# Performance work log

Hardware: AMD Instinct MI355X
Metric: run time of the kernel (lower is better)

Reference implementation:

```python
import jax, jax.numpy as jnp
import numpy as np

D_MODEL = 1024
NHEAD = 16
HEAD_DIM = D_MODEL // NHEAD
LN_EPS = 1e-5
ROPE_BASE = 10000.0


def _rope_cos_sin(n, head_dim):
    inv_freq = 1.0 / (ROPE_BASE ** (jnp.arange(0, head_dim, 2, dtype=jnp.float32) / head_dim))
    t = jnp.arange(n, dtype=jnp.float32)
    freqs = jnp.outer(t, inv_freq)  # (N, head_dim//2)
    return jnp.cos(freqs), jnp.sin(freqs)


def _apply_rope(x, cos, sin):
    # x: (B, H, N, hd); cos/sin: (N, hd//2)
    B, H, N, hd = x.shape
    xr = x.reshape(B, H, N, hd // 2, 2)
    x0, x1 = xr[..., 0], xr[..., 1]
    c = cos[None, None]
    s = sin[None, None]
    rot = jnp.stack([x0 * c - x1 * s, x0 * s + x1 * c], axis=-1)
    return rot.reshape(B, H, N, hd)


def setup_inputs() -> dict:
    key = jax.random.key(0)
    ks = jax.random.split(key, 6)
    D = D_MODEL
    scale = 1.0 / np.sqrt(D)
    x = jax.random.normal(ks[0], (2, 2048, D), dtype=jnp.float32)
    Wq = jax.random.normal(ks[1], (D, D), dtype=jnp.float32) * scale
    Wk = jax.random.normal(ks[2], (D, D), dtype=jnp.float32) * scale
    Wv = jax.random.normal(ks[3], (D, D), dtype=jnp.float32) * scale
    Wo = jax.random.normal(ks[4], (D, D), dtype=jnp.float32) * scale
    bq = jnp.zeros((D,), jnp.float32)
    bk = jnp.zeros((D,), jnp.float32)
    bv = jnp.zeros((D,), jnp.float32)
    bo = jnp.zeros((D,), jnp.float32)
    ln_w = jnp.ones((D,), jnp.float32)
    ln_b = jnp.zeros((D,), jnp.float32)
    return {"x": x, "ln_w": ln_w, "ln_b": ln_b, "Wq": Wq, "bq": bq,
            "Wk": Wk, "bk": bk, "Wv": Wv, "bv": bv, "Wo": Wo, "bo": bo}


def reference(x, ln_w, ln_b, Wq, bq, Wk, bk, Wv, bv, Wo, bo):
    B, N, D = x.shape
    H, hd = NHEAD, HEAD_DIM
    # LayerNorm
    mu = jnp.mean(x, axis=-1, keepdims=True)
    var = jnp.mean(jnp.square(x - mu), axis=-1, keepdims=True)
    xn = (x - mu) * jax.lax.rsqrt(var + LN_EPS) * ln_w + ln_b
    # QKV projections -> (B, H, N, hd)
    def proj(W, b):
        return (xn @ W.T + b).reshape(B, N, H, hd).transpose(0, 2, 1, 3)
    q = proj(Wq, bq)
    k = proj(Wk, bk)
    v = proj(Wv, bv)
    cos, sin = _rope_cos_sin(N, hd)
    q = _apply_rope(q, cos, sin)
    k = _apply_rope(k, cos, sin)
    scores = jnp.einsum('bhqd,bhkd->bhqk', q, k) / jnp.sqrt(jnp.float32(hd))
    attn = jax.nn.softmax(scores, axis=-1)
    out = jnp.einsum('bhqk,bhkd->bhqd', attn, v)
    out = out.transpose(0, 2, 1, 3).reshape(B, N, D)
    return x + out @ Wo.T + bo
```

## Files before the change

### kernel.cpp

```cpp
#include <hip/hip_runtime.h>


#define SEQ 2048
#define LN_EPS 1e-5f

using short8 = __attribute__((ext_vector_type(8))) short;
using f32x4  = __attribute__((ext_vector_type(4))) float;

__device__ __forceinline__ unsigned short f2bf(float f) {
  union { float f; unsigned u; } v; v.f = f;
  unsigned r = v.u + 0x7FFFu + ((v.u >> 16) & 1u);
  return (unsigned short)(r >> 16);
}

__device__ __forceinline__ void async16(const void* g, void* l) {
  __builtin_amdgcn_global_load_lds(
      (const __attribute__((address_space(1))) void*)g,
      (__attribute__((address_space(3))) void*)l, 16, 0, 0);
}

__global__ __launch_bounds__(256) void prep_kernel(
    const float* __restrict__ x, const float* __restrict__ lnw, const float* __restrict__ lnb,
    const float* __restrict__ wq, const float* __restrict__ wk,
    const float* __restrict__ wv, const float* __restrict__ wo,
    unsigned short* __restrict__ wqkv, unsigned short* __restrict__ wob,
    unsigned short* __restrict__ xn, float2* __restrict__ tab) {
  const int b = blockIdx.x, t = threadIdx.x;
  if (b < 4096) {
    const int gid = b * 256 + t;
    const int m = gid >> 18, e4 = gid & 262143;
    const float* src = (m == 0) ? wq : (m == 1) ? wk : (m == 2) ? wv : wo;
    const float4 v = ((const float4*)src)[e4];
    ushort4 o; o.x = f2bf(v.x); o.y = f2bf(v.y); o.z = f2bf(v.z); o.w = f2bf(v.w);
    if (m < 3) ((ushort4*)wqkv)[(size_t)m * 262144 + e4] = o;
    else       ((ushort4*)wob)[e4] = o;
  } else if (b < 8192) {
    const int row = b - 4096;
    const float4 v = ((const float4*)(x + (size_t)row * 1024))[t];
    float s  = v.x + v.y + v.z + v.w;
    float s2 = v.x * v.x + v.y * v.y + v.z * v.z + v.w * v.w;
#pragma unroll
    for (int off = 32; off >= 1; off >>= 1) {
      s  += __shfl_xor(s, off);
      s2 += __shfl_xor(s2, off);
    }
    __shared__ float red[8];
    const int lane = t & 63, wave = t >> 6;
    if (lane == 0) { red[wave] = s; red[4 + wave] = s2; }
    __syncthreads();
    s  = red[0] + red[1] + red[2] + red[3];
    s2 = red[4] + red[5] + red[6] + red[7];
    const float mu   = s * (1.0f / 1024.0f);
    const float var  = s2 * (1.0f / 1024.0f) - mu * mu;
    const float rstd = rsqrtf(var + LN_EPS);
    const float4 wv4 = ((const float4*)lnw)[t];
    const float4 bv4 = ((const float4*)lnb)[t];
    ushort4 o;
    o.x = f2bf((v.x - mu) * rstd * wv4.x + bv4.x);
    o.y = f2bf((v.y - mu) * rstd * wv4.y + bv4.y);
    o.z = f2bf((v.z - mu) * rstd * wv4.z + bv4.z);
    o.w = f2bf((v.w - mu) * rstd * wv4.w + bv4.w);
    ((ushort4*)xn)[(size_t)row * 256 + t] = o;
  } else {
    const int gid = (b - 8192) * 256 + t;
    const int pos = gid >> 5, ip = gid & 31;
    const float invf = exp2f((float)ip * -0.4152410118609203f);
    const float fr = (float)pos * invf;
    tab[gid] = make_float2(cosf(fr), sinf(fr));
  }
}

__global__ __launch_bounds__(256, 3) void gemm_kernel(
    const unsigned short* __restrict__ A,
    const unsigned short* __restrict__ Bw,
    int mode,
    const float* __restrict__ bq, const float* __restrict__ bk, const float* __restrict__ bv,
    const float2* __restrict__ tab,
    unsigned short* __restrict__ qb, unsigned short* __restrict__ kbg,
    unsigned short* __restrict__ vtb,
    const float* __restrict__ bo, const float* __restrict__ xres, float* __restrict__ out) {
  __shared__ unsigned short lA[128 * 64];
  __shared__ unsigned short lB[128 * 64];
  const int tid = threadIdx.x;
  const int lane = tid & 63, wave = tid >> 6;
  const int lr = lane & 15, quad = lane >> 4;
  const int wm = (wave >> 1) * 64, wn = (wave & 1) * 64;
  const int n0 = blockIdx.x * 128, m0 = blockIdx.y * 128;
  const int r7 = lr & 7;
  const int lrow = lane >> 3, lcg = (lane & 7) ^ lrow;

  f32x4 acc[4][4];
#pragma unroll
  for (int i = 0; i < 4; ++i)
#pragma unroll
    for (int j = 0; j < 4; ++j) acc[i][j] = (f32x4){0.f, 0.f, 0.f, 0.f};

  for (int kt = 0; kt < 16; ++kt) {
    __syncthreads();
#pragma unroll
    for (int c = 0; c < 4; ++c) {
      const int chunk = wave * 4 + c;
      const int grow = chunk * 8 + lrow;
      async16(&A[(size_t)(m0 + grow) * 1024 + kt * 64 + lcg * 8], &lA[chunk * 512]);
      async16(&Bw[(size_t)(n0 + grow) * 1024 + kt * 64 + lcg * 8], &lB[chunk * 512]);
    }
    __syncthreads();
#pragma unroll
    for (int kk = 0; kk < 2; ++kk) {
      short8 a[4], b[4];
#pragma unroll
      for (int i = 0; i < 4; ++i)
        a[i] = *(const short8*)&lA[(wm + i * 16 + lr) * 64 + ((kk * 4 + quad) ^ r7) * 8];
#pragma unroll
      for (int j = 0; j < 4; ++j)
        b[j] = *(const short8*)&lB[(wn + j * 16 + lr) * 64 + ((kk * 4 + quad) ^ r7) * 8];
#pragma unroll
      for (int i = 0; i < 4; ++i)
#pragma unroll
        for (int j = 0; j < 4; ++j)
          acc[i][j] = __builtin_amdgcn_mfma_f32_16x16x32_bf16(a[i], b[j], acc[i][j], 0, 0, 0);
    }
  }

  if (mode == 0) {
    const int which = n0 >> 10;
    const float* bias = (which == 0) ? bq : (which == 1) ? bk : bv;
    const float qs = (which == 0) ? 0.18033688011112042f : 1.0f;
#pragma unroll
    for (int i = 0; i < 4; ++i)
#pragma unroll
      for (int j = 0; j < 4; ++j)
#pragma unroll
        for (int r = 0; r < 4; ++r) {
          const int row = m0 + wm + i * 16 + quad * 4 + r;
          const int col = n0 + wn + j * 16 + lr;
          const int c = col & 1023;
          float val = (acc[i][j][r] + bias[c]) * qs;
          const int head = c >> 6, hd_i = c & 63;
          const int b_ = row >> 11, pos = row & 2047;
          if (which < 2) {
            const float partner = __shfl_xor(val, 1);
            const float2 cs = tab[(pos << 5) + (hd_i >> 1)];
            val = val * cs.x + partner * ((lane & 1) ? cs.y : -cs.y);
          }
          if (which == 2) {
            vtb[((size_t)((b_ * 16 + head) * 64 + hd_i)) * SEQ + pos] = f2bf(val);
          } else {
            const size_t didx = ((size_t)((b_ * 16 + head) * SEQ + pos)) * 64 + hd_i;
            if (which == 0) qb[didx] = f2bf(val);
            else            kbg[didx] = f2bf(val);
          }
        }
  } else {
#pragma unroll
    for (int i = 0; i < 4; ++i)
#pragma unroll
      for (int j = 0; j < 4; ++j)
#pragma unroll
        for (int r = 0; r < 4; ++r) {
          const int row = m0 + wm + i * 16 + quad * 4 + r;
          const int col = n0 + wn + j * 16 + lr;
          const size_t idx = (size_t)row * 1024 + col;
          out[idx] = acc[i][j][r] + bo[col] + xres[idx];
        }
  }
}

__global__ __launch_bounds__(256) void attn_kernel(
    const unsigned short* __restrict__ qg, const unsigned short* __restrict__ kg,
    const unsigned short* __restrict__ vtg, unsigned short* __restrict__ ao) {
  __shared__ unsigned short lK[128 * 64];
  __shared__ unsigned short lV[64 * 128];
  __shared__ unsigned short lP[4][32 * 128];
  const int tid = threadIdx.x;
  const int lane = tid & 63, w = tid >> 6;
  const int lr = lane & 15, quad = lane >> 4;
  const int r7 = lr & 7;
  const int bh = blockIdx.x >> 4, qt = blockIdx.x & 15;
  const int q0 = qt * 128 + w * 32;
  const unsigned short* Q  = qg + (size_t)bh * SEQ * 64;
  const unsigned short* K  = kg + (size_t)bh * SEQ * 64;
  const unsigned short* VT = vtg + (size_t)bh * 64 * SEQ;
  unsigned short* lPw = lP[w];

  short8 qf[2][2];
#pragma unroll
  for (int t = 0; t < 2; ++t)
#pragma unroll
    for (int kk = 0; kk < 2; ++kk)
      qf[t][kk] = *(const short8*)&Q[(size_t)(q0 + t * 16 + lr) * 64 + kk * 32 + quad * 8];

  short8 onesf;
  {
    const short o1 = (lr == 0) ? (short)0x3F80 : (short)0;
#pragma unroll
    for (int j = 0; j < 8; ++j) onesf[j] = o1;
  }

  f32x4 o[2][4], ol[2];
#pragma unroll
  for (int t = 0; t < 2; ++t) {
    ol[t] = (f32x4){0.f, 0.f, 0.f, 0.f};
#pragma unroll
    for (int d = 0; d < 4; ++d) o[t][d] = (f32x4){0.f, 0.f, 0.f, 0.f};
  }

  const int k_row = lane >> 3, k_g = (lane & 7) ^ (k_row & 7);
  const int v_row = lane >> 4, v_g0 = lane & 15;

  for (int kt = 0; kt < 16; ++kt) {
    __syncthreads();
#pragma unroll
    for (int c = 0; c < 4; ++c) {
      const int kc = w * 4 + c;
      const int krow = kc * 8 + k_row;
      async16(&K[(size_t)(kt * 128 + krow) * 64 + k_g * 8], &lK[kc * 512]);
      const int vc = w * 4 + c;
      const int vrow = vc * 4 + v_row;
      const int vg = v_g0 ^ (vrow & 7);
      async16(&VT[(size_t)vrow * SEQ + kt * 128 + vg * 8], &lV[vc * 512]);
    }
    __syncthreads();

#pragma unroll
    for (int kb = 0; kb < 8; ++kb) {
      const short8 k0 = *(const short8*)&lK[(kb * 16 + lr) * 64 + (quad ^ r7) * 8];
      const short8 k1 = *(const short8*)&lK[(kb * 16 + lr) * 64 + ((4 + quad) ^ r7) * 8];
#pragma unroll
      for (int t = 0; t < 2; ++t) {
        f32x4 st = (f32x4){0.f, 0.f, 0.f, 0.f};
        st = __builtin_amdgcn_mfma_f32_16x16x32_bf16(k0, qf[t][0], st, 0, 0, 0);
        st = __builtin_amdgcn_mfma_f32_16x16x32_bf16(k1, qf[t][1], st, 0, 0, 0);
        union { float f; unsigned u; } c0, c1, c2, c3;
        c0.f = __builtin_amdgcn_exp2f(st[0]);
        c1.f = __builtin_amdgcn_exp2f(st[1]);
        c2.f = __builtin_amdgcn_exp2f(st[2]);
        c3.f = __builtin_amdgcn_exp2f(st[3]);
        uint2 pw;
        pw.x = __builtin_amdgcn_perm(c1.u, c0.u, 0x07060302u);
        pw.y = __builtin_amdgcn_perm(c3.u, c2.u, 0x07060302u);
        *(uint2*)&lPw[(t * 16 + lr) * 128 + ((kb * 2 + (quad >> 1)) ^ r7) * 8 + (quad & 1) * 4] = pw;
      }
    }
    __asm__ __volatile__("s_waitcnt lgkmcnt(0)" ::: "memory");

#pragma unroll
    for (int k2 = 0; k2 < 4; ++k2) {
      const short8 pf0 = *(const short8*)&lPw[lr * 128 + ((k2 * 4 + quad) ^ r7) * 8];
      const short8 pf1 = *(const short8*)&lPw[(16 + lr) * 128 + ((k2 * 4 + quad) ^ r7) * 8];
      ol[0] = __builtin_amdgcn_mfma_f32_16x16x32_bf16(pf0, onesf, ol[0], 0, 0, 0);
      ol[1] = __builtin_amdgcn_mfma_f32_16x16x32_bf16(pf1, onesf, ol[1], 0, 0, 0);
#pragma unroll
      for (int d = 0; d < 4; ++d) {
        const short8 vf = *(const short8*)&lV[(d * 16 + lr) * 128 + ((k2 * 4 + quad) ^ r7) * 8];
        o[0][d] = __builtin_amdgcn_mfma_f32_16x16x32_bf16(pf0, vf, o[0][d], 0, 0, 0);
        o[1][d] = __builtin_amdgcn_mfma_f32_16x16x32_bf16(pf1, vf, o[1][d], 0, 0, 0);
      }
    }
  }

  const int b_ = bh >> 4, h = bh & 15;
#pragma unroll
  for (int t = 0; t < 2; ++t)
#pragma unroll
    for (int r = 0; r < 4; ++r) {
      const float l = __shfl(ol[t][r], lane & 48);
      const float rl = 1.0f / l;
#pragma unroll
      for (int d = 0; d < 4; ++d) {
        const int row = q0 + t * 16 + quad * 4 + r;
        ao[(size_t)(b_ * SEQ + row) * 1024 + h * 64 + d * 16 + lr] = f2bf(o[t][d][r] * rl);
      }
    }
}

extern "C" void kernel_launch(void* const* d_in, const int* in_sizes, int n_in,
                              void* d_out, int out_size, void* d_ws, size_t ws_size,
                              hipStream_t stream) {
  const float* x   = (const float*)d_in[0];
  const float* lnw = (const float*)d_in[1];
  const float* lnb = (const float*)d_in[2];
  const float* Wq  = (const float*)d_in[3];
  const float* bq  = (const float*)d_in[4];
  const float* Wk  = (const float*)d_in[5];
  const float* bk  = (const float*)d_in[6];
  const float* Wv  = (const float*)d_in[7];
  const float* bv  = (const float*)d_in[8];
  const float* Wo  = (const float*)d_in[9];
  const float* bo  = (const float*)d_in[10];
  float* out = (float*)d_out;

  char* ws = (char*)d_ws;
  unsigned short* wqkv = (unsigned short*)(ws);
  unsigned short* wob  = (unsigned short*)(ws + 6291456);
  unsigned short* xn   = (unsigned short*)(ws + 8388608);
  unsigned short* qb   = (unsigned short*)(ws + 16777216);
  unsigned short* kbuf = (unsigned short*)(ws + 25165824);
  unsigned short* vtb  = (unsigned short*)(ws + 33554432);
  unsigned short* ao   = (unsigned short*)(ws + 41943040);
  float2*         tab  = (float2*)(ws + 50331648);

  hipLaunchKernelGGL(prep_kernel, dim3(8448), dim3(256), 0, stream,
                     x, lnw, lnb, Wq, Wk, Wv, Wo, wqkv, wob, xn, tab);
  hipLaunchKernelGGL(gemm_kernel, dim3(24, 32), dim3(256), 0, stream,
                     xn, wqkv, 0, bq, bk, bv, tab, qb, kbuf, vtb,
                     (const float*)nullptr, (const float*)nullptr, (float*)nullptr);
  hipLaunchKernelGGL(attn_kernel, dim3(512), dim3(256), 0, stream, qb, kbuf, vtb, ao);
  hipLaunchKernelGGL(gemm_kernel, dim3(8, 32), dim3(256), 0, stream,
                     ao, wob, 1,
                     (const float*)nullptr, (const float*)nullptr, (const float*)nullptr, tab,
                     (unsigned short*)nullptr, (unsigned short*)nullptr, (unsigned short*)nullptr,
                     bo, x, out);
}
```

Measured before the change: 223.2 us.

## Split GEMM kernels, halve O-projection tile width, stagger K-loop start per block wave

```diff
diff --git a/kernel.cpp b/kernel.cpp
--- a/kernel.cpp
+++ b/kernel.cpp
@@ -70,15 +70,13 @@
   }
 }
 
-__global__ __launch_bounds__(256, 3) void gemm_kernel(
+__global__ __launch_bounds__(256, 3) void gemm_qkv_kernel(
     const unsigned short* __restrict__ A,
     const unsigned short* __restrict__ Bw,
-    int mode,
     const float* __restrict__ bq, const float* __restrict__ bk, const float* __restrict__ bv,
     const float2* __restrict__ tab,
     unsigned short* __restrict__ qb, unsigned short* __restrict__ kbg,
-    unsigned short* __restrict__ vtb,
-    const float* __restrict__ bo, const float* __restrict__ xres, float* __restrict__ out) {
+    unsigned short* __restrict__ vtb) {
   __shared__ unsigned short lA[128 * 64];
   __shared__ unsigned short lB[128 * 64];
   const int tid = threadIdx.x;
@@ -88,6 +86,8 @@
   const int n0 = blockIdx.x * 128, m0 = blockIdx.y * 128;
   const int r7 = lr & 7;
   const int lrow = lane >> 3, lcg = (lane & 7) ^ lrow;
+  const int lin = blockIdx.y * gridDim.x + blockIdx.x;
+  const int phase = ((lin >> 8) * 5) & 15;
 
   f32x4 acc[4][4];
 #pragma unroll
@@ -96,13 +96,14 @@
     for (int j = 0; j < 4; ++j) acc[i][j] = (f32x4){0.f, 0.f, 0.f, 0.f};
 
   for (int kt = 0; kt < 16; ++kt) {
+    const int kofs = ((kt + phase) & 15) * 64;
     __syncthreads();
 #pragma unroll
     for (int c = 0; c < 4; ++c) {
       const int chunk = wave * 4 + c;
       const int grow = chunk * 8 + lrow;
-      async16(&A[(size_t)(m0 + grow) * 1024 + kt * 64 + lcg * 8], &lA[chunk * 512]);
-      async16(&Bw[(size_t)(n0 + grow) * 1024 + kt * 64 + lcg * 8], &lB[chunk * 512]);
+      async16(&A[(size_t)(m0 + grow) * 1024 + kofs + lcg * 8], &lA[chunk * 512]);
+      async16(&Bw[(size_t)(n0 + grow) * 1024 + kofs + lcg * 8], &lB[chunk * 512]);
     }
     __syncthreads();
 #pragma unroll
@@ -122,48 +123,102 @@
     }
   }
 
-  if (mode == 0) {
-    const int which = n0 >> 10;
-    const float* bias = (which == 0) ? bq : (which == 1) ? bk : bv;
-    const float qs = (which == 0) ? 0.18033688011112042f : 1.0f;
-#pragma unroll
-    for (int i = 0; i < 4; ++i)
-#pragma unroll
-      for (int j = 0; j < 4; ++j)
-#pragma unroll
-        for (int r = 0; r < 4; ++r) {
-          const int row = m0 + wm + i * 16 + quad * 4 + r;
-          const int col = n0 + wn + j * 16 + lr;
-          const int c = col & 1023;
-          float val = (acc[i][j][r] + bias[c]) * qs;
-          const int head = c >> 6, hd_i = c & 63;
-          const int b_ = row >> 11, pos = row & 2047;
-          if (which < 2) {
-            const float partner = __shfl_xor(val, 1);
-            const float2 cs = tab[(pos << 5) + (hd_i >> 1)];
-            val = val * cs.x + partner * ((lane & 1) ? cs.y : -cs.y);
-          }
-          if (which == 2) {
-            vtb[((size_t)((b_ * 16 + head) * 64 + hd_i)) * SEQ + pos] = f2bf(val);
-          } else {
-            const size_t didx = ((size_t)((b_ * 16 + head) * SEQ + pos)) * 64 + hd_i;
-            if (which == 0) qb[didx] = f2bf(val);
-            else            kbg[didx] = f2bf(val);
-          }
+  const int which = n0 >> 10;
+  const float* bias = (which == 0) ? bq : (which == 1) ? bk : bv;
+  const float qs = (which == 0) ? 0.18033688011112042f : 1.0f;
+#pragma unroll
+  for (int i = 0; i < 4; ++i)
+#pragma unroll
+    for (int j = 0; j < 4; ++j)
+#pragma unroll
+      for (int r = 0; r < 4; ++r) {
+        const int row = m0 + wm + i * 16 + quad * 4 + r;
+        const int col = n0 + wn + j * 16 + lr;
+        const int c = col & 1023;
+        float val = (acc[i][j][r] + bias[c]) * qs;
+        const int head = c >> 6, hd_i = c & 63;
+        const int b_ = row >> 11, pos = row & 2047;
+        if (which < 2) {
+          const float partner = __shfl_xor(val, 1);
+          const float2 cs = tab[(pos << 5) + (hd_i >> 1)];
+          val = val * cs.x + partner * ((lane & 1) ? cs.y : -cs.y);
         }
-  } else {
-#pragma unroll
-    for (int i = 0; i < 4; ++i)
-#pragma unroll
-      for (int j = 0; j < 4; ++j)
-#pragma unroll
-        for (int r = 0; r < 4; ++r) {
-          const int row = m0 + wm + i * 16 + quad * 4 + r;
-          const int col = n0 + wn + j * 16 + lr;
-          const size_t idx = (size_t)row * 1024 + col;
-          out[idx] = acc[i][j][r] + bo[col] + xres[idx];
+        if (which == 2) {
+          vtb[((size_t)((b_ * 16 + head) * 64 + hd_i)) * SEQ + pos] = f2bf(val);
+        } else {
+          const size_t didx = ((size_t)((b_ * 16 + head) * SEQ + pos)) * 64 + hd_i;
+          if (which == 0) qb[didx] = f2bf(val);
+          else            kbg[didx] = f2bf(val);
         }
-  }
+      }
+}
+
+__global__ __launch_bounds__(256, 3) void gemm_o_kernel(
+    const unsigned short* __restrict__ A,
+    const unsigned short* __restrict__ Bw,
+    const float* __restrict__ bo, const float* __restrict__ xres, float* __restrict__ out) {
+  __shared__ unsigned short lA[128 * 64];
+  __shared__ unsigned short lB[64 * 64];
+  const int tid = threadIdx.x;
+  const int lane = tid & 63, wave = tid >> 6;
+  const int lr = lane & 15, quad = lane >> 4;
+  const int wm = (wave >> 1) * 64, wn = (wave & 1) * 32;
+  const int n0 = blockIdx.x * 64, m0 = blockIdx.y * 128;
+  const int r7 = lr & 7;
+  const int lrow = lane >> 3, lcg = (lane & 7) ^ lrow;
+  const int lin = blockIdx.y * gridDim.x + blockIdx.x;
+  const int phase = ((lin >> 8) * 8) & 15;
+
+  f32x4 acc[4][2];
+#pragma unroll
+  for (int i = 0; i < 4; ++i)
+#pragma unroll
+    for (int j = 0; j < 2; ++j) acc[i][j] = (f32x4){0.f, 0.f, 0.f, 0.f};
+
+  for (int kt = 0; kt < 16; ++kt) {
+    const int kofs = ((kt + phase) & 15) * 64;
+    __syncthreads();
+#pragma unroll
+    for (int c = 0; c < 4; ++c) {
+      const int chunk = wave * 4 + c;
+      const int grow = chunk * 8 + lrow;
+      async16(&A[(size_t)(m0 + grow) * 1024 + kofs + lcg * 8], &lA[chunk * 512]);
+    }
+#pragma unroll
+    for (int c = 0; c < 2; ++c) {
+      const int chunk = wave * 2 + c;
+      const int grow = chunk * 8 + lrow;
+      async16(&Bw[(size_t)(n0 + grow) * 1024 + kofs + lcg * 8], &lB[chunk * 512]);
+    }
+    __syncthreads();
+#pragma unroll
+    for (int kk = 0; kk < 2; ++kk) {
+      short8 a[4], b[2];
+#pragma unroll
+      for (int i = 0; i < 4; ++i)
+        a[i] = *(const short8*)&lA[(wm + i * 16 + lr) * 64 + ((kk * 4 + quad) ^ r7) * 8];
+#pragma unroll
+      for (int j = 0; j < 2; ++j)
+        b[j] = *(const short8*)&lB[(wn + j * 16 + lr) * 64 + ((kk * 4 + quad) ^ r7) * 8];
+#pragma unroll
+      for (int i = 0; i < 4; ++i)
+#pragma unroll
+        for (int j = 0; j < 2; ++j)
+          acc[i][j] = __builtin_amdgcn_mfma_f32_16x16x32_bf16(a[i], b[j], acc[i][j], 0, 0, 0);
+    }
+  }
+
+#pragma unroll
+  for (int i = 0; i < 4; ++i)
+#pragma unroll
+    for (int j = 0; j < 2; ++j)
+#pragma unroll
+      for (int r = 0; r < 4; ++r) {
+        const int row = m0 + wm + i * 16 + quad * 4 + r;
+        const int col = n0 + wn + j * 16 + lr;
+        const size_t idx = (size_t)row * 1024 + col;
+        out[idx] = acc[i][j][r] + bo[col] + xres[idx];
+      }
 }
 
 __global__ __launch_bounds__(256) void attn_kernel(
@@ -178,6 +233,7 @@
   const int r7 = lr & 7;
   const int bh = blockIdx.x >> 4, qt = blockIdx.x & 15;
   const int q0 = qt * 128 + w * 32;
+  const int phase = ((blockIdx.x >> 8) * 8) & 15;
   const unsigned short* Q  = qg + (size_t)bh * SEQ * 64;
   const unsigned short* K  = kg + (size_t)bh * SEQ * 64;
   const unsigned short* VT = vtg + (size_t)bh * 64 * SEQ;
@@ -209,16 +265,17 @@
   const int v_row = lane >> 4, v_g0 = lane & 15;
 
   for (int kt = 0; kt < 16; ++kt) {
+    const int kb0 = ((kt + phase) & 15) * 128;
     __syncthreads();
 #pragma unroll
     for (int c = 0; c < 4; ++c) {
       const int kc = w * 4 + c;
       const int krow = kc * 8 + k_row;
-      async16(&K[(size_t)(kt * 128 + krow) * 64 + k_g * 8], &lK[kc * 512]);
+      async16(&K[(size_t)(kb0 + krow) * 64 + k_g * 8], &lK[kc * 512]);
       const int vc = w * 4 + c;
       const int vrow = vc * 4 + v_row;
       const int vg = v_g0 ^ (vrow & 7);
-      async16(&VT[(size_t)vrow * SEQ + kt * 128 + vg * 8], &lV[vc * 512]);
+      async16(&VT[(size_t)vrow * SEQ + kb0 + vg * 8], &lV[vc * 512]);
     }
     __syncthreads();
 
@@ -302,13 +359,9 @@
 
   hipLaunchKernelGGL(prep_kernel, dim3(8448), dim3(256), 0, stream,
                      x, lnw, lnb, Wq, Wk, Wv, Wo, wqkv, wob, xn, tab);
-  hipLaunchKernelGGL(gemm_kernel, dim3(24, 32), dim3(256), 0, stream,
-                     xn, wqkv, 0, bq, bk, bv, tab, qb, kbuf, vtb,
-                     (const float*)nullptr, (const float*)nullptr, (float*)nullptr);
+  hipLaunchKernelGGL(gemm_qkv_kernel, dim3(24, 32), dim3(256), 0, stream,
+                     xn, wqkv, bq, bk, bv, tab, qb, kbuf, vtb);
   hipLaunchKernelGGL(attn_kernel, dim3(512), dim3(256), 0, stream, qb, kbuf, vtb, ao);
-  hipLaunchKernelGGL(gemm_kernel, dim3(8, 32), dim3(256), 0, stream,
-                     ao, wob, 1,
-                     (const float*)nullptr, (const float*)nullptr, (const float*)nullptr, tab,
-                     (unsigned short*)nullptr, (unsigned short*)nullptr, (unsigned short*)nullptr,
-                     bo, x, out);
-}
+  hipLaunchKernelGGL(gemm_o_kernel, dim3(16, 32), dim3(256), 0, stream,
+                     ao, wob, bo, x, out);
+}
```

New measurement: 211.4 us. 5.3% less time.
